# Kernel tuning notes

Hardware: AMD Instinct MI355X
Metric: run time of the kernel (lower is better)

The kernel has to match this reference:

```python
import jax, jax.numpy as jnp
import numpy as np

B, S, D, H, L, FF = 4, 2048, 256, 8, 4, 512
DK = D // H
EPS = 1e-5


def _ln(x, scale, bias):
    m = jnp.mean(x, axis=-1, keepdims=True)
    v = jnp.mean(jnp.square(x - m), axis=-1, keepdims=True)
    return (x - m) / jnp.sqrt(v + EPS) * scale + bias


def setup_inputs() -> dict:
    key = jax.random.key(0)
    ks = jax.random.split(key, 12)
    w = lambda k, shape: jax.random.normal(k, shape, dtype=jnp.float32) * 0.02
    return {
        "x": jax.random.normal(ks[0], (B, S, D), dtype=jnp.float32),
        "ln0_s": jnp.ones((D,), jnp.float32), "ln0_b": jnp.zeros((D,), jnp.float32),
        "ln1_s": jnp.ones((L, D), jnp.float32), "ln1_b": jnp.zeros((L, D), jnp.float32),
        "ln2_s": jnp.ones((L, D), jnp.float32), "ln2_b": jnp.zeros((L, D), jnp.float32),
        "wq": w(ks[1], (L, D, D)), "bq": jnp.zeros((L, D), jnp.float32),
        "wk": w(ks[2], (L, D, D)), "bk": jnp.zeros((L, D), jnp.float32),
        "wv": w(ks[3], (L, D, D)), "bv": jnp.zeros((L, D), jnp.float32),
        "wo": w(ks[4], (L, D, D)), "bo": jnp.zeros((L, D), jnp.float32),
        "w1": w(ks[5], (L, D, FF)), "b1": jnp.zeros((L, FF), jnp.float32),
        "w2": w(ks[6], (L, FF, D)), "b2": jnp.zeros((L, D), jnp.float32),
    }


def reference(x, ln0_s, ln0_b, ln1_s, ln1_b, ln2_s, ln2_b,
              wq, bq, wk, bk, wv, bv, wo, bo, w1, b1, w2, b2):
    scale = 1.0 / np.sqrt(DK).astype(np.float32)
    x = _ln(x, ln0_s, ln0_b)  # Encoder's leading LayerNorm

    def step(h, p):
        (l1s, l1b, l2s, l2b, Wq, Bq, Wk, Bk, Wv, Bv, Wo, Bo, W1, B1, W2, B2) = p
        # --- pre-norm multi-head attention ---
        x2 = _ln(h, l1s, l1b)
        q = (x2 @ Wq + Bq).reshape(B, S, H, DK)
        k = (x2 @ Wk + Bk).reshape(B, S, H, DK)
        v = (x2 @ Wv + Bv).reshape(B, S, H, DK)
        scores = jnp.einsum('bqhd,bkhd->bhqk', q, k) * scale  # [B,H,S,S]
        attn = jax.nn.softmax(scores, axis=-1)
        o = jnp.einsum('bhqk,bkhd->bqhd', attn, v).reshape(B, S, D)
        h = h + (o @ Wo + Bo)
        # --- pre-norm feed-forward (hidden fixed at 512, ReLU) ---
        x2 = _ln(h, l2s, l2b)
        h = h + (jax.nn.relu(x2 @ W1 + B1) @ W2 + B2)
        return h, None

    layer_params = (ln1_s, ln1_b, ln2_s, ln2_b, wq, bq, wk, bk,
                    wv, bv, wo, bo, w1, b1, w2, b2)
    x, _ = jax.lax.scan(step, x, layer_params)
    return x
```

## Files before the change

kernel.cpp:

```cpp
#include <hip/hip_runtime.h>
#include <hip/hip_bf16.h>
#include <math.h>

#define SEQ 2048
#define DIM 256
#define NH 8
#define DK 32
#define FF 512

typedef __bf16 bf16_t;
typedef bf16_t bf16x8 __attribute__((ext_vector_type(8)));
typedef bf16_t bf16x4 __attribute__((ext_vector_type(4)));
typedef float f32x4 __attribute__((ext_vector_type(4)));

#define QK_SCALE_LOG2 0.25503226632462494f
#if __has_builtin(__builtin_amdgcn_exp2f)
#define FAST_EXP2(x) __builtin_amdgcn_exp2f(x)
#else
#define FAST_EXP2(x) __expf((x) * 0.6931471805599453f)
#endif

__global__ __launch_bounds__(256) void ln_double_kernel(
    const float* __restrict__ x, const float* __restrict__ s0,
    const float* __restrict__ b0, const float* __restrict__ s1,
    const float* __restrict__ b1, float* __restrict__ outf,
    bf16_t* __restrict__ outb) {
  int wave = threadIdx.x >> 6;
  int lane = threadIdx.x & 63;
  int row = blockIdx.x * 4 + wave;
  float4 xv = *(const float4*)(x + (size_t)row * DIM + lane * 4);
  float sum = xv.x + xv.y + xv.z + xv.w;
  float sq = xv.x * xv.x + xv.y * xv.y + xv.z * xv.z + xv.w * xv.w;
#pragma unroll
  for (int off = 1; off < 64; off <<= 1) {
    sum += __shfl_xor(sum, off);
    sq += __shfl_xor(sq, off);
  }
  float mean = sum * (1.0f / 256.0f);
  float var = sq * (1.0f / 256.0f) - mean * mean;
  float inv = rsqrtf(var + 1e-5f);
  float4 sv = *(const float4*)(s0 + lane * 4);
  float4 bv = *(const float4*)(b0 + lane * 4);
  float4 h;
  h.x = (xv.x - mean) * inv * sv.x + bv.x;
  h.y = (xv.y - mean) * inv * sv.y + bv.y;
  h.z = (xv.z - mean) * inv * sv.z + bv.z;
  h.w = (xv.w - mean) * inv * sv.w + bv.w;
  *(float4*)(outf + (size_t)row * DIM + lane * 4) = h;
  float sum2 = h.x + h.y + h.z + h.w;
  float sq2 = h.x * h.x + h.y * h.y + h.z * h.z + h.w * h.w;
#pragma unroll
  for (int off = 1; off < 64; off <<= 1) {
    sum2 += __shfl_xor(sum2, off);
    sq2 += __shfl_xor(sq2, off);
  }
  float mean2 = sum2 * (1.0f / 256.0f);
  float var2 = sq2 * (1.0f / 256.0f) - mean2 * mean2;
  float inv2 = rsqrtf(var2 + 1e-5f);
  float4 s1v = *(const float4*)(s1 + lane * 4);
  float4 b1v = *(const float4*)(b1 + lane * 4);
  bf16x4 ob = {(bf16_t)((h.x - mean2) * inv2 * s1v.x + b1v.x),
               (bf16_t)((h.y - mean2) * inv2 * s1v.y + b1v.y),
               (bf16_t)((h.z - mean2) * inv2 * s1v.z + b1v.z),
               (bf16_t)((h.w - mean2) * inv2 * s1v.w + b1v.w)};
  *(bf16x4*)(outb + (size_t)row * DIM + lane * 4) = ob;
}

__global__ __launch_bounds__(256) void wtrans_all_kernel(
    const float* __restrict__ wq, const float* __restrict__ wk,
    const float* __restrict__ wv, const float* __restrict__ wo,
    const float* __restrict__ w1, const float* __restrict__ w2,
    bf16_t* __restrict__ WqT, bf16_t* __restrict__ WkT,
    bf16_t* __restrict__ WvT, bf16_t* __restrict__ WoT,
    bf16_t* __restrict__ W1T, bf16_t* __restrict__ W2T) {
  __shared__ float tile[64][65];
  int idx = blockIdx.x;
  int layer = idx >> 7;
  int r = idx & 127;
  const float* src;
  bf16_t* dst;
  int N, k0, n0;
  if (r < 64) {
    int which = r >> 4, t = r & 15;
    N = 256;
    k0 = (t & 3) * 64;
    n0 = (t >> 2) * 64;
    src = (which == 0 ? wq : which == 1 ? wk : which == 2 ? wv : wo) + (size_t)layer * 65536;
    dst = (which == 0 ? WqT : which == 1 ? WkT : which == 2 ? WvT : WoT) + (size_t)layer * 65536;
  } else if (r < 96) {
    int t = r - 64;
    N = 512;
    k0 = (t & 3) * 64;
    n0 = (t >> 2) * 64;
    src = w1 + (size_t)layer * 131072;
    dst = W1T + (size_t)layer * 131072;
  } else {
    int t = r - 96;
    N = 256;
    k0 = (t & 7) * 64;
    n0 = (t >> 3) * 64;
    src = w2 + (size_t)layer * 131072;
    dst = W2T + (size_t)layer * 131072;
  }
  int K = (r >= 96) ? 512 : 256;

  int tr = threadIdx.x >> 4;
  int tc4 = (threadIdx.x & 15) * 4;
#pragma unroll
  for (int i = 0; i < 4; i++) {
    int kl = i * 16 + tr;
    float4 v = *(const float4*)(src + (size_t)(k0 + kl) * N + n0 + tc4);
    tile[kl][tc4 + 0] = v.x; tile[kl][tc4 + 1] = v.y;
    tile[kl][tc4 + 2] = v.z; tile[kl][tc4 + 3] = v.w;
  }
  __syncthreads();
#pragma unroll
  for (int i = 0; i < 4; i++) {
    int nl = i * 16 + tr;
    bf16x4 o = {(bf16_t)tile[tc4 + 0][nl], (bf16_t)tile[tc4 + 1][nl],
                (bf16_t)tile[tc4 + 2][nl], (bf16_t)tile[tc4 + 3][nl]};
    *(bf16x4*)(dst + (size_t)(n0 + nl) * K + k0 + tc4) = o;
  }
}

__device__ __forceinline__ void stage128(const bf16_t* __restrict__ src,
                                         bf16_t* dst, int tid, int ldk, int k0) {
#pragma unroll
  for (int u = 0; u < 4; u++) {
    int i = u * 256 + tid;
    int m = i >> 3, cd = i & 7, cs = cd ^ (m & 7);
    __builtin_amdgcn_global_load_lds(
        (const __attribute__((address_space(1))) unsigned int*)(src + (size_t)m * ldk + k0 + cs * 8),
        (__attribute__((address_space(3))) unsigned int*)(dst + i * 8), 16, 0, 0);
  }
}

__device__ __forceinline__ void stage256(const bf16_t* __restrict__ src,
                                         bf16_t* dst, int tid, int ldk, int k0) {
#pragma unroll
  for (int u = 0; u < 8; u++) {
    int j = u * 256 + tid;
    int m = j >> 3, cd = j & 7, cs = cd ^ (m & 7);
    __builtin_amdgcn_global_load_lds(
        (const __attribute__((address_space(1))) unsigned int*)(src + (size_t)m * ldk + k0 + cs * 8),
        (__attribute__((address_space(3))) unsigned int*)(dst + j * 8), 16, 0, 0);
  }
}

__device__ __forceinline__ void compute128(const bf16_t* As, const bf16_t* Bs,
                                           int wr, int wc, int n16, int quad,
                                           f32x4 (&acc)[4][4]) {
#pragma unroll
  for (int ks = 0; ks < 2; ks++) {
    bf16x8 af[4], bf[4];
#pragma unroll
    for (int mt = 0; mt < 4; mt++) {
      int row = wr * 64 + mt * 16 + n16;
      int cd = (ks * 4 + quad) ^ (row & 7);
      af[mt] = *(const bf16x8*)(As + row * 64 + cd * 8);
    }
#pragma unroll
    for (int nt = 0; nt < 4; nt++) {
      int row = wc * 64 + nt * 16 + n16;
      int cd = (ks * 4 + quad) ^ (row & 7);
      bf[nt] = *(const bf16x8*)(Bs + row * 64 + cd * 8);
    }
#pragma unroll
    for (int mt = 0; mt < 4; mt++)
#pragma unroll
      for (int nt = 0; nt < 4; nt++)
        acc[mt][nt] = __builtin_amdgcn_mfma_f32_16x16x32_bf16(
            af[mt], bf[nt], acc[mt][nt], 0, 0, 0);
  }
}

template <int K>
__device__ __forceinline__ void gemm9_body(
    const bf16_t* __restrict__ A, const bf16_t* __restrict__ BT,
    int m0, int n0, int tid, bf16_t* As, bf16_t* Bs, f32x4 (&acc)[4][4]) {
  int lane = tid & 63;
  int n16 = lane & 15, quad = lane >> 4;
  int w = tid >> 6;
  int wr = w >> 1, wc = w & 1;
  const bf16_t* Arow = A + (size_t)m0 * K;
  const bf16_t* Brow = BT + (size_t)n0 * K;

  stage128(Arow, As, tid, K, 0);
  stage128(Brow, Bs, tid, K, 0);

  const int steps = K / 64;
#pragma unroll
  for (int s = 0; s < steps; s++) {
    int buf = s & 1;
    if (s + 1 < steps) {
      stage128(Arow, As + (buf ^ 1) * 8192, tid, K, (s + 1) * 64);
      stage128(Brow, Bs + (buf ^ 1) * 8192, tid, K, (s + 1) * 64);
    }
    __syncthreads();
    compute128(As + buf * 8192, Bs + buf * 8192, wr, wc, n16, quad, acc);
    if (s + 2 < steps) __syncthreads();
  }
}

__global__ __launch_bounds__(256) void qkv9_kernel(
    const bf16_t* __restrict__ A,
    const bf16_t* __restrict__ WqT, const bf16_t* __restrict__ WkT,
    const bf16_t* __restrict__ WvT,
    const float* __restrict__ bq, const float* __restrict__ bk,
    const float* __restrict__ bv,
    bf16_t* __restrict__ qo, bf16_t* __restrict__ ko,
    bf16_t* __restrict__ vo) {
  __shared__ __align__(16) bf16_t As[2 * 8192];
  __shared__ __align__(16) bf16_t Bs[2 * 8192];
  int which = blockIdx.x >> 1;
  int nblk = blockIdx.x & 1;
  const bf16_t* BT = (which == 0) ? WqT : (which == 1) ? WkT : WvT;
  const float* bias = (which == 0) ? bq : (which == 1) ? bk : bv;

  int tid = threadIdx.x;
  int lane = tid & 63;
  int n16 = lane & 15, quad = lane >> 4;
  int w = tid >> 6;
  int wr = w >> 1, wc = w & 1;
  int m0 = blockIdx.y * 128, n0 = nblk * 128;
  f32x4 acc[4][4] = {};
  gemm9_body<256>(A, BT, m0, n0, tid, As, Bs, acc);

#pragma unroll
  for (int nt = 0; nt < 4; nt++) {
    int n = n0 + wc * 64 + nt * 16 + n16;
    float bv_ = bias[n];
    int hh = n >> 5, dk = n & 31;
#pragma unroll
    for (int mt = 0; mt < 4; mt++) {
      if (which == 2) {
        int s0 = m0 + wr * 64 + mt * 16 + quad * 4;
        int bb = s0 >> 11, ss0 = s0 & 2047;
        bf16x4 o;
#pragma unroll
        for (int r = 0; r < 4; r++) o[r] = (bf16_t)(acc[mt][nt][r] + bv_);
        *(bf16x4*)(vo + ((size_t)(bb * NH + hh) * DK + dk) * SEQ + ss0) = o;
      } else {
        bf16_t* dst = (which == 0) ? qo : ko;
        float sc = (which == 0) ? QK_SCALE_LOG2 : 1.0f;
#pragma unroll
        for (int r = 0; r < 4; r++) {
          int m = m0 + wr * 64 + mt * 16 + quad * 4 + r;
          int bb = m >> 11, ss = m & 2047;
          dst[((size_t)(bb * NH + hh) * SEQ + ss) * DK + dk] =
              (bf16_t)((acc[mt][nt][r] + bv_) * sc);
        }
      }
    }
  }
}

template <int K, int LNOUT>
__global__ __launch_bounds__(256) void gemm_ln_kernel(
    const bf16_t* __restrict__ A, const bf16_t* __restrict__ BT,
    const float* __restrict__ bias, const float* __restrict__ resid,
    float* __restrict__ outf, const float* __restrict__ ls,
    const float* __restrict__ lb, bf16_t* __restrict__ outb) {
  __shared__ __align__(16) bf16_t As[2 * 2048];
  __shared__ __align__(16) bf16_t Bs[2 * 16384];
  __shared__ float2 stats[4][32];
  int tid = threadIdx.x;
  int lane = tid & 63;
  int n16 = lane & 15, quad = lane >> 4;
  int w = tid >> 6;
  int m0 = blockIdx.x * 32;

  const bf16_t* Arow = A + (size_t)m0 * K;
  f32x4 acc[2][4] = {};

  {
    int i = tid;
    int m = i >> 3, cd = i & 7, cs = cd ^ (m & 7);
    __builtin_amdgcn_global_load_lds(
        (const __attribute__((address_space(1))) unsigned int*)(Arow + (size_t)m * K + cs * 8),
        (__attribute__((address_space(3))) unsigned int*)(As + i * 8), 16, 0, 0);
    stage256(BT, Bs, tid, K, 0);
  }

  const int steps = K / 64;
#pragma unroll
  for (int s = 0; s < steps; s++) {
    int buf = s & 1;
    if (s + 1 < steps) {
      int k0 = (s + 1) * 64;
      int i = tid;
      int m = i >> 3, cd = i & 7, cs = cd ^ (m & 7);
      __builtin_amdgcn_global_load_lds(
          (const __attribute__((address_space(1))) unsigned int*)(Arow + (size_t)m * K + k0 + cs * 8),
          (__attribute__((address_space(3))) unsigned int*)(As + (buf ^ 1) * 2048 + i * 8), 16, 0, 0);
      stage256(BT, Bs + (buf ^ 1) * 16384, tid, K, k0);
    }
    __syncthreads();
    const bf16_t* a = As + buf * 2048;
    const bf16_t* b = Bs + buf * 16384;
#pragma unroll
    for (int ks = 0; ks < 2; ks++) {
      bf16x8 af[2], bfv[4];
#pragma unroll
      for (int mt = 0; mt < 2; mt++) {
        int row = mt * 16 + n16;
        int cd = (ks * 4 + quad) ^ (row & 7);
        af[mt] = *(const bf16x8*)(a + row * 64 + cd * 8);
      }
#pragma unroll
      for (int nt = 0; nt < 4; nt++) {
        int row = w * 64 + nt * 16 + n16;
        int cd = (ks * 4 + quad) ^ (row & 7);
        bfv[nt] = *(const bf16x8*)(b + row * 64 + cd * 8);
      }
#pragma unroll
      for (int mt = 0; mt < 2; mt++)
#pragma unroll
        for (int nt = 0; nt < 4; nt++)
          acc[mt][nt] = __builtin_amdgcn_mfma_f32_16x16x32_bf16(
              af[mt], bfv[nt], acc[mt][nt], 0, 0, 0);
    }
    if (s + 2 < steps) __syncthreads();
  }

  float rsum[2][4], rsq[2][4];
#pragma unroll
  for (int mt = 0; mt < 2; mt++)
#pragma unroll
    for (int r = 0; r < 4; r++) { rsum[mt][r] = 0.f; rsq[mt][r] = 0.f; }

#pragma unroll
  for (int nt = 0; nt < 4; nt++) {
    int n = w * 64 + nt * 16 + n16;
    float bv = bias[n];
#pragma unroll
    for (int mt = 0; mt < 2; mt++)
#pragma unroll
      for (int r = 0; r < 4; r++) {
        int m = m0 + mt * 16 + quad * 4 + r;
        size_t idx = (size_t)m * DIM + n;
        float hv = resid[idx] + acc[mt][nt][r] + bv;
        outf[idx] = hv;
        acc[mt][nt][r] = hv;
        rsum[mt][r] += hv;
        rsq[mt][r] += hv * hv;
      }
  }

  if (LNOUT) {
#pragma unroll
    for (int mt = 0; mt < 2; mt++)
#pragma unroll
      for (int r = 0; r < 4; r++) {
        float s_ = rsum[mt][r], q_ = rsq[mt][r];
#pragma unroll
        for (int off = 1; off < 16; off <<= 1) {
          s_ += __shfl_xor(s_, off);
          q_ += __shfl_xor(q_, off);
        }
        rsum[mt][r] = s_;
        rsq[mt][r] = q_;
      }
    if (n16 == 0) {
#pragma unroll
      for (int mt = 0; mt < 2; mt++)
#pragma unroll
        for (int r = 0; r < 4; r++)
          stats[w][mt * 16 + quad * 4 + r] = make_float2(rsum[mt][r], rsq[mt][r]);
    }
    __syncthreads();
#pragma unroll
    for (int mt = 0; mt < 2; mt++)
#pragma unroll
      for (int r = 0; r < 4; r++) {
        int lr = mt * 16 + quad * 4 + r;
        float2 t0 = stats[0][lr], t1 = stats[1][lr], t2 = stats[2][lr], t3 = stats[3][lr];
        float tot = t0.x + t1.x + t2.x + t3.x;
        float totq = t0.y + t1.y + t2.y + t3.y;
        float mean = tot * (1.0f / 256.0f);
        float var = totq * (1.0f / 256.0f) - mean * mean;
        rsum[mt][r] = mean;
        rsq[mt][r] = rsqrtf(var + 1e-5f);
      }
#pragma unroll
    for (int nt = 0; nt < 4; nt++) {
      int n = w * 64 + nt * 16 + n16;
      float sv = ls[n], bv = lb[n];
#pragma unroll
      for (int mt = 0; mt < 2; mt++)
#pragma unroll
        for (int r = 0; r < 4; r++) {
          int m = m0 + mt * 16 + quad * 4 + r;
          float x2 = (acc[mt][nt][r] - rsum[mt][r]) * rsq[mt][r] * sv + bv;
          outb[(size_t)m * DIM + n] = (bf16_t)x2;
        }
    }
  }
}

template <int LNOUT>
__global__ __launch_bounds__(256) void ffn_kernel(
    const bf16_t* __restrict__ x2, const bf16_t* __restrict__ W1T,
    const bf16_t* __restrict__ W2T, const float* __restrict__ b1,
    const float* __restrict__ b2, const float* __restrict__ resid,
    float* __restrict__ outf, const float* __restrict__ ls,
    const float* __restrict__ lb, bf16_t* __restrict__ outb) {
  __shared__ __align__(16) bf16_t Wbuf[2][16384];
  __shared__ __align__(16) bf16_t H1s[32 * 512];
  __shared__ float2 stats[4][32];
  int tid = threadIdx.x;
  int lane = tid & 63;
  int n16 = lane & 15, quad = lane >> 4;
  int w = tid >> 6;
  int m0 = blockIdx.x * 32;

#pragma unroll
  for (int s = 0; s < 2; s++) {
    const bf16_t* Wsrc = W1T + (size_t)s * 256 * 256;
    f32x4 acc_a[4][2] = {};
    stage256(Wsrc, Wbuf[0], tid, 256, 0);
#pragma unroll
    for (int t = 0; t < 4; t++) {
      int buf = t & 1;
      if (t + 1 < 4) stage256(Wsrc, Wbuf[buf ^ 1], tid, 256, (t + 1) * 64);
      __syncthreads();
#pragma unroll
      for (int ks = 0; ks < 2; ks++) {
        bf16x8 af[4];
#pragma unroll
        for (int mt = 0; mt < 4; mt++) {
          int row = w * 64 + mt * 16 + n16;
          int cd = (ks * 4 + quad) ^ (row & 7);
          af[mt] = *(const bf16x8*)(Wbuf[buf] + row * 64 + cd * 8);
        }
        bf16x8 xf[2];
#pragma unroll
        for (int nt = 0; nt < 2; nt++)
          xf[nt] = *(const bf16x8*)(x2 + (size_t)(m0 + nt * 16 + n16) * 256 +
                                    t * 64 + ks * 32 + quad * 8);
#pragma unroll
        for (int mt = 0; mt < 4; mt++)
#pragma unroll
          for (int nt = 0; nt < 2; nt++)
            acc_a[mt][nt] = __builtin_amdgcn_mfma_f32_16x16x32_bf16(
                af[mt], xf[nt], acc_a[mt][nt], 0, 0, 0);
      }
      __syncthreads();
    }
#pragma unroll
    for (int mt = 0; mt < 4; mt++) {
      int hid0 = s * 256 + w * 64 + mt * 16 + quad * 4;
      float b1v0 = b1[hid0], b1v1 = b1[hid0 + 1], b1v2 = b1[hid0 + 2], b1v3 = b1[hid0 + 3];
      int c = hid0 >> 3;
      int off4 = (quad & 1) * 4;
#pragma unroll
      for (int nt = 0; nt < 2; nt++) {
        int tok = nt * 16 + n16;
        bf16x4 o = {(bf16_t)fmaxf(acc_a[mt][nt][0] + b1v0, 0.0f),
                    (bf16_t)fmaxf(acc_a[mt][nt][1] + b1v1, 0.0f),
                    (bf16_t)fmaxf(acc_a[mt][nt][2] + b1v2, 0.0f),
                    (bf16_t)fmaxf(acc_a[mt][nt][3] + b1v3, 0.0f)};
        int cs = c ^ (n16 & 7);
        *(bf16x4*)(H1s + tok * 512 + cs * 8 + off4) = o;
      }
    }
  }
  __syncthreads();

  f32x4 acc[2][4] = {};
  stage256(W2T, Wbuf[0], tid, 512, 0);
#pragma unroll
  for (int s = 0; s < 8; s++) {
    int buf = s & 1;
    if (s + 1 < 8) stage256(W2T, Wbuf[buf ^ 1], tid, 512, (s + 1) * 64);
    __syncthreads();
#pragma unroll
    for (int ks = 0; ks < 2; ks++) {
      bf16x8 af2[2];
#pragma unroll
      for (int mt = 0; mt < 2; mt++) {
        int tok = mt * 16 + n16;
        int g = (s * 8 + ks * 4 + quad) ^ (n16 & 7);
        af2[mt] = *(const bf16x8*)(H1s + tok * 512 + g * 8);
      }
      bf16x8 bf2[4];
#pragma unroll
      for (int nt = 0; nt < 4; nt++) {
        int rowb = w * 64 + nt * 16 + n16;
        int cd = (ks * 4 + quad) ^ (rowb & 7);
        bf2[nt] = *(const bf16x8*)(Wbuf[buf] + rowb * 64 + cd * 8);
      }
#pragma unroll
      for (int mt = 0; mt < 2; mt++)
#pragma unroll
        for (int nt = 0; nt < 4; nt++)
          acc[mt][nt] = __builtin_amdgcn_mfma_f32_16x16x32_bf16(
              af2[mt], bf2[nt], acc[mt][nt], 0, 0, 0);
    }
    __syncthreads();
  }

  float rsum[2][4], rsq[2][4];
#pragma unroll
  for (int mt = 0; mt < 2; mt++)
#pragma unroll
    for (int r = 0; r < 4; r++) { rsum[mt][r] = 0.f; rsq[mt][r] = 0.f; }

#pragma unroll
  for (int nt = 0; nt < 4; nt++) {
    int n = w * 64 + nt * 16 + n16;
    float bv = b2[n];
#pragma unroll
    for (int mt = 0; mt < 2; mt++)
#pragma unroll
      for (int r = 0; r < 4; r++) {
        int m = m0 + mt * 16 + quad * 4 + r;
        size_t idx = (size_t)m * DIM + n;
        float hv = resid[idx] + acc[mt][nt][r] + bv;
        outf[idx] = hv;
        acc[mt][nt][r] = hv;
        rsum[mt][r] += hv;
        rsq[mt][r] += hv * hv;
      }
  }

  if (LNOUT) {
#pragma unroll
    for (int mt = 0; mt < 2; mt++)
#pragma unroll
      for (int r = 0; r < 4; r++) {
        float s_ = rsum[mt][r], q_ = rsq[mt][r];
#pragma unroll
        for (int off = 1; off < 16; off <<= 1) {
          s_ += __shfl_xor(s_, off);
          q_ += __shfl_xor(q_, off);
        }
        rsum[mt][r] = s_;
        rsq[mt][r] = q_;
      }
    if (n16 == 0) {
#pragma unroll
      for (int mt = 0; mt < 2; mt++)
#pragma unroll
        for (int r = 0; r < 4; r++)
          stats[w][mt * 16 + quad * 4 + r] = make_float2(rsum[mt][r], rsq[mt][r]);
    }
    __syncthreads();
#pragma unroll
    for (int mt = 0; mt < 2; mt++)
#pragma unroll
      for (int r = 0; r < 4; r++) {
        int lr = mt * 16 + quad * 4 + r;
        float2 t0 = stats[0][lr], t1 = stats[1][lr], t2 = stats[2][lr], t3 = stats[3][lr];
        float tot = t0.x + t1.x + t2.x + t3.x;
        float totq = t0.y + t1.y + t2.y + t3.y;
        float mean = tot * (1.0f / 256.0f);
        float var = totq * (1.0f / 256.0f) - mean * mean;
        rsum[mt][r] = mean;
        rsq[mt][r] = rsqrtf(var + 1e-5f);
      }
#pragma unroll
    for (int nt = 0; nt < 4; nt++) {
      int n = w * 64 + nt * 16 + n16;
      float sv = ls[n], bv = lb[n];
#pragma unroll
      for (int mt = 0; mt < 2; mt++)
#pragma unroll
        for (int r = 0; r < 4; r++) {
          int m = m0 + mt * 16 + quad * 4 + r;
          float x2v = (acc[mt][nt][r] - rsum[mt][r]) * rsq[mt][r] * sv + bv;
          outb[(size_t)m * DIM + n] = (bf16_t)x2v;
        }
    }
  }
}

__global__ __launch_bounds__(128) void flash8_kernel(
    const bf16_t* __restrict__ Q, const bf16_t* __restrict__ K,
    const bf16_t* __restrict__ VT, bf16_t* __restrict__ OB) {
  __shared__ __align__(16) bf16_t Plds[2][2][32][72];
  int bh = blockIdx.x;
  int q0 = blockIdx.y * 64;
  int w = threadIdx.x >> 6;
  int lane = threadIdx.x & 63;
  int n16 = lane & 15;
  int quad = lane >> 4;

  const bf16_t* Qb = Q + (size_t)bh * SEQ * DK;
  const bf16_t* Kb = K + (size_t)bh * SEQ * DK;
  const bf16_t* Vb = VT + (size_t)bh * DK * SEQ;
  int qr0 = q0 + w * 32;

  bf16x8 qfrag[2];
#pragma unroll
  for (int qg = 0; qg < 2; qg++)
    qfrag[qg] = *(const bf16x8*)(Qb + (size_t)(qr0 + qg * 16 + n16) * DK + quad * 8);

  bf16_t one = (bf16_t)1.0f;
  bf16x8 ones = {one, one, one, one, one, one, one, one};

  f32x4 oacc[2][2] = {};
  f32x4 lacc[2] = {};

  {
    bf16x8 kf0[4];
#pragma unroll
    for (int t = 0; t < 4; t++)
      kf0[t] = *(const bf16x8*)(Kb + (size_t)(t * 16 + n16) * DK + quad * 8);
#pragma unroll
    for (int qg = 0; qg < 2; qg++)
#pragma unroll
      for (int t = 0; t < 4; t++) {
        f32x4 sc = __builtin_amdgcn_mfma_f32_16x16x32_bf16(
            kf0[t], qfrag[qg], (f32x4){0.f, 0.f, 0.f, 0.f}, 0, 0, 0);
        bf16x4 pf;
#pragma unroll
        for (int r = 0; r < 4; r++) pf[r] = (bf16_t)FAST_EXP2(sc[r]);
        *(bf16x4*)&Plds[0][w][qg * 16 + n16][t * 16 + quad * 4] = pf;
      }
  }
  bf16x8 kfS[4], vfP[2][2];
#pragma unroll
  for (int t = 0; t < 4; t++)
    kfS[t] = *(const bf16x8*)(Kb + (size_t)(64 + t * 16 + n16) * DK + quad * 8);
#pragma unroll
  for (int c = 0; c < 2; c++) {
    vfP[c][0] = *(const bf16x8*)(Vb + (size_t)n16 * SEQ + c * 32 + quad * 8);
    vfP[c][1] = *(const bf16x8*)(Vb + (size_t)(16 + n16) * SEQ + c * 32 + quad * 8);
  }

#pragma unroll 2
  for (int i = 0; i < 32; i++) {
    int buf = i & 1;
    bf16x8 pf8[2][2];
#pragma unroll
    for (int qg = 0; qg < 2; qg++)
#pragma unroll
      for (int c = 0; c < 2; c++)
        pf8[qg][c] = *(const bf16x8*)&Plds[buf][w][qg * 16 + n16][c * 32 + quad * 8];
    bf16x8 kfN[4], vfN[2][2];
    if (i + 2 < 32) {
      int kb = (i + 2) * 64;
#pragma unroll
      for (int t = 0; t < 4; t++)
        kfN[t] = *(const bf16x8*)(Kb + (size_t)(kb + t * 16 + n16) * DK + quad * 8);
    }
    if (i + 1 < 32) {
      int kb = (i + 1) * 64;
#pragma unroll
      for (int c = 0; c < 2; c++) {
        vfN[c][0] = *(const bf16x8*)(Vb + (size_t)n16 * SEQ + kb + c * 32 + quad * 8);
        vfN[c][1] = *(const bf16x8*)(Vb + (size_t)(16 + n16) * SEQ + kb + c * 32 + quad * 8);
      }
    }
    if (i + 1 < 32) {
#pragma unroll
      for (int qg = 0; qg < 2; qg++)
#pragma unroll
        for (int t = 0; t < 4; t++) {
          f32x4 sc = __builtin_amdgcn_mfma_f32_16x16x32_bf16(
              kfS[t], qfrag[qg], (f32x4){0.f, 0.f, 0.f, 0.f}, 0, 0, 0);
          bf16x4 pf;
#pragma unroll
          for (int r = 0; r < 4; r++) pf[r] = (bf16_t)FAST_EXP2(sc[r]);
          *(bf16x4*)&Plds[buf ^ 1][w][qg * 16 + n16][t * 16 + quad * 4] = pf;
        }
    }
#pragma unroll
    for (int qg = 0; qg < 2; qg++)
#pragma unroll
      for (int c = 0; c < 2; c++) {
        lacc[qg] = __builtin_amdgcn_mfma_f32_16x16x32_bf16(pf8[qg][c], ones, lacc[qg], 0, 0, 0);
        oacc[qg][0] = __builtin_amdgcn_mfma_f32_16x16x32_bf16(pf8[qg][c], vfP[c][0], oacc[qg][0], 0, 0, 0);
        oacc[qg][1] = __builtin_amdgcn_mfma_f32_16x16x32_bf16(pf8[qg][c], vfP[c][1], oacc[qg][1], 0, 0, 0);
      }
    if (i + 2 < 32) {
#pragma unroll
      for (int t = 0; t < 4; t++) kfS[t] = kfN[t];
    }
    if (i + 1 < 32) {
#pragma unroll
      for (int c = 0; c < 2; c++) {
        vfP[c][0] = vfN[c][0];
        vfP[c][1] = vfN[c][1];
      }
    }
  }

  int bb = bh >> 3, hh = bh & 7;
#pragma unroll
  for (int qg = 0; qg < 2; qg++)
#pragma unroll
    for (int r = 0; r < 4; r++) {
      float linv = 1.0f / lacc[qg][r];
      int row = qr0 + qg * 16 + quad * 4 + r;
      bf16_t* op = OB + ((size_t)(bb * SEQ + row)) * DIM + hh * DK;
      op[n16] = (bf16_t)(oacc[qg][0][r] * linv);
      op[16 + n16] = (bf16_t)(oacc[qg][1][r] * linv);
    }
}

extern "C" void kernel_launch(void* const* d_in, const int* in_sizes, int n_in,
                              void* d_out, int out_size, void* d_ws, size_t ws_size,
                              hipStream_t stream) {
  const float* x     = (const float*)d_in[0];
  const float* ln0_s = (const float*)d_in[1];
  const float* ln0_b = (const float*)d_in[2];
  const float* ln1_s = (const float*)d_in[3];
  const float* ln1_b = (const float*)d_in[4];
  const float* ln2_s = (const float*)d_in[5];
  const float* ln2_b = (const float*)d_in[6];
  const float* wq = (const float*)d_in[7];
  const float* bq = (const float*)d_in[8];
  const float* wk = (const float*)d_in[9];
  const float* bk = (const float*)d_in[10];
  const float* wv = (const float*)d_in[11];
  const float* bv = (const float*)d_in[12];
  const float* wo = (const float*)d_in[13];
  const float* bo = (const float*)d_in[14];
  const float* w1 = (const float*)d_in[15];
  const float* b1 = (const float*)d_in[16];
  const float* w2 = (const float*)d_in[17];
  const float* b2 = (const float*)d_in[18];

  float* out = (float*)d_out;
  const size_t ACT = (size_t)8192 * DIM;

  bf16_t* wsb = (bf16_t*)d_ws;
  bf16_t* x2b = wsb;
  bf16_t* obf = x2b + ACT;
  bf16_t* qbf = obf + ACT;
  bf16_t* kbf = qbf + ACT;
  bf16_t* vbf = kbf + ACT;
  bf16_t* WqT = vbf + ACT;
  bf16_t* WkT = WqT + 4 * 65536;
  bf16_t* WvT = WkT + 4 * 65536;
  bf16_t* WoT = WvT + 4 * 65536;
  bf16_t* W1T = WoT + 4 * 65536;
  bf16_t* W2T = W1T + 4 * 131072;

  dim3 blk(256);
  dim3 blkF(128);
  dim3 gLN(2048);
  dim3 gRow(256);
  dim3 gQKV(6, 64);
  dim3 gAtt(32, 32);

  wtrans_all_kernel<<<dim3(512), blk, 0, stream>>>(wq, wk, wv, wo, w1, w2,
                                                   WqT, WkT, WvT, WoT, W1T, W2T);

  ln_double_kernel<<<gLN, blk, 0, stream>>>(x, ln0_s, ln0_b, ln1_s, ln1_b, out, x2b);

  for (int l = 0; l < 4; l++) {
    bf16_t* WqTl = WqT + (size_t)l * 65536;
    bf16_t* WkTl = WkT + (size_t)l * 65536;
    bf16_t* WvTl = WvT + (size_t)l * 65536;
    bf16_t* WoTl = WoT + (size_t)l * 65536;
    bf16_t* W1Tl = W1T + (size_t)l * 131072;
    bf16_t* W2Tl = W2T + (size_t)l * 131072;

    qkv9_kernel<<<gQKV, blk, 0, stream>>>(x2b, WqTl, WkTl, WvTl,
                                          bq + l * DIM, bk + l * DIM, bv + l * DIM,
                                          qbf, kbf, vbf);
    flash8_kernel<<<gAtt, blkF, 0, stream>>>(qbf, kbf, vbf, obf);
    gemm_ln_kernel<256, 1><<<gRow, blk, 0, stream>>>(
        obf, WoTl, bo + l * DIM, out, out, ln2_s + l * DIM, ln2_b + l * DIM, x2b);
    if (l < 3) {
      ffn_kernel<1><<<gRow, blk, 0, stream>>>(
          x2b, W1Tl, W2Tl, b1 + l * FF, b2 + l * DIM, out, out,
          ln1_s + (l + 1) * DIM, ln1_b + (l + 1) * DIM, x2b);
    } else {
      ffn_kernel<0><<<gRow, blk, 0, stream>>>(
          x2b, W1Tl, W2Tl, b1 + l * FF, b2 + l * DIM, out, out,
          nullptr, nullptr, nullptr);
    }
  }
}
```

Measured before the change: 453.0 us.

## Split attention key range across two blocks and combine partial results

```diff
diff --git a/kernel.cpp b/kernel.cpp
--- a/kernel.cpp
+++ b/kernel.cpp
@@ -575,20 +575,22 @@
   }
 }
 
-__global__ __launch_bounds__(128) void flash8_kernel(
+__global__ __launch_bounds__(128, 4) void flash9_kernel(
     const bf16_t* __restrict__ Q, const bf16_t* __restrict__ K,
-    const bf16_t* __restrict__ VT, bf16_t* __restrict__ OB) {
+    const bf16_t* __restrict__ VT, float* __restrict__ Opart,
+    float* __restrict__ lpart) {
   __shared__ __align__(16) bf16_t Plds[2][2][32][72];
   int bh = blockIdx.x;
   int q0 = blockIdx.y * 64;
+  int part = blockIdx.z;
   int w = threadIdx.x >> 6;
   int lane = threadIdx.x & 63;
   int n16 = lane & 15;
   int quad = lane >> 4;
 
   const bf16_t* Qb = Q + (size_t)bh * SEQ * DK;
-  const bf16_t* Kb = K + (size_t)bh * SEQ * DK;
-  const bf16_t* Vb = VT + (size_t)bh * DK * SEQ;
+  const bf16_t* Kb = K + (size_t)bh * SEQ * DK + (size_t)part * 1024 * DK;
+  const bf16_t* Vb = VT + (size_t)bh * DK * SEQ + part * 1024;
   int qr0 = q0 + w * 32;
 
   bf16x8 qfrag[2];
@@ -630,7 +632,7 @@
   }
 
 #pragma unroll 2
-  for (int i = 0; i < 32; i++) {
+  for (int i = 0; i < 16; i++) {
     int buf = i & 1;
     bf16x8 pf8[2][2];
 #pragma unroll
@@ -639,13 +641,13 @@
       for (int c = 0; c < 2; c++)
         pf8[qg][c] = *(const bf16x8*)&Plds[buf][w][qg * 16 + n16][c * 32 + quad * 8];
     bf16x8 kfN[4], vfN[2][2];
-    if (i + 2 < 32) {
+    if (i + 2 < 16) {
       int kb = (i + 2) * 64;
 #pragma unroll
       for (int t = 0; t < 4; t++)
         kfN[t] = *(const bf16x8*)(Kb + (size_t)(kb + t * 16 + n16) * DK + quad * 8);
     }
-    if (i + 1 < 32) {
+    if (i + 1 < 16) {
       int kb = (i + 1) * 64;
 #pragma unroll
       for (int c = 0; c < 2; c++) {
@@ -653,7 +655,7 @@
         vfN[c][1] = *(const bf16x8*)(Vb + (size_t)(16 + n16) * SEQ + kb + c * 32 + quad * 8);
       }
     }
-    if (i + 1 < 32) {
+    if (i + 1 < 16) {
 #pragma unroll
       for (int qg = 0; qg < 2; qg++)
 #pragma unroll
@@ -674,11 +676,11 @@
         oacc[qg][0] = __builtin_amdgcn_mfma_f32_16x16x32_bf16(pf8[qg][c], vfP[c][0], oacc[qg][0], 0, 0, 0);
         oacc[qg][1] = __builtin_amdgcn_mfma_f32_16x16x32_bf16(pf8[qg][c], vfP[c][1], oacc[qg][1], 0, 0, 0);
       }
-    if (i + 2 < 32) {
+    if (i + 2 < 16) {
 #pragma unroll
       for (int t = 0; t < 4; t++) kfS[t] = kfN[t];
     }
-    if (i + 1 < 32) {
+    if (i + 1 < 16) {
 #pragma unroll
       for (int c = 0; c < 2; c++) {
         vfP[c][0] = vfN[c][0];
@@ -687,17 +689,34 @@
     }
   }
 
+  size_t rowbase = (size_t)part * 65536 + (size_t)bh * SEQ;
+#pragma unroll
+  for (int qg = 0; qg < 2; qg++) {
+#pragma unroll
+    for (int r = 0; r < 4; r++) {
+      int row = qr0 + qg * 16 + quad * 4 + r;
+      float* op = Opart + (rowbase + row) * 32;
+      op[n16] = oacc[qg][0][r];
+      op[16 + n16] = oacc[qg][1][r];
+      if (n16 == 0) lpart[rowbase + row] = lacc[qg][r];
+    }
+  }
+}
+
+__global__ __launch_bounds__(256) void combine_kernel(
+    const float* __restrict__ Opart, const float* __restrict__ lpart,
+    bf16_t* __restrict__ OB) {
+  int g = blockIdx.x * 256 + threadIdx.x;
+  int row = g >> 3;
+  int dk0 = (g & 7) * 4;
+  float4 o0 = *(const float4*)(Opart + (size_t)row * 32 + dk0);
+  float4 o1 = *(const float4*)(Opart + (size_t)(65536 + row) * 32 + dk0);
+  float linv = 1.0f / (lpart[row] + lpart[65536 + row]);
+  int bh = row >> 11, s = row & 2047;
   int bb = bh >> 3, hh = bh & 7;
-#pragma unroll
-  for (int qg = 0; qg < 2; qg++)
-#pragma unroll
-    for (int r = 0; r < 4; r++) {
-      float linv = 1.0f / lacc[qg][r];
-      int row = qr0 + qg * 16 + quad * 4 + r;
-      bf16_t* op = OB + ((size_t)(bb * SEQ + row)) * DIM + hh * DK;
-      op[n16] = (bf16_t)(oacc[qg][0][r] * linv);
-      op[16 + n16] = (bf16_t)(oacc[qg][1][r] * linv);
-    }
+  bf16x4 o = {(bf16_t)((o0.x + o1.x) * linv), (bf16_t)((o0.y + o1.y) * linv),
+              (bf16_t)((o0.z + o1.z) * linv), (bf16_t)((o0.w + o1.w) * linv)};
+  *(bf16x4*)(OB + ((size_t)(bb * SEQ + s)) * DIM + hh * DK + dk0) = o;
 }
 
 extern "C" void kernel_launch(void* const* d_in, const int* in_sizes, int n_in,
@@ -738,13 +757,16 @@
   bf16_t* WoT = WvT + 4 * 65536;
   bf16_t* W1T = WoT + 4 * 65536;
   bf16_t* W2T = W1T + 4 * 131072;
+  float* Opart = (float*)(W2T + 4 * 131072);
+  float* lpart = Opart + (size_t)2 * 65536 * 32;
 
   dim3 blk(256);
   dim3 blkF(128);
   dim3 gLN(2048);
   dim3 gRow(256);
   dim3 gQKV(6, 64);
-  dim3 gAtt(32, 32);
+  dim3 gAtt(32, 32, 2);
+  dim3 gComb(2048);
 
   wtrans_all_kernel<<<dim3(512), blk, 0, stream>>>(wq, wk, wv, wo, w1, w2,
                                                    WqT, WkT, WvT, WoT, W1T, W2T);
@@ -762,7 +784,8 @@
     qkv9_kernel<<<gQKV, blk, 0, stream>>>(x2b, WqTl, WkTl, WvTl,
                                           bq + l * DIM, bk + l * DIM, bv + l * DIM,
                                           qbf, kbf, vbf);
-    flash8_kernel<<<gAtt, blkF, 0, stream>>>(qbf, kbf, vbf, obf);
+    flash9_kernel<<<gAtt, blkF, 0, stream>>>(qbf, kbf, vbf, Opart, lpart);
+    combine_kernel<<<gComb, blk, 0, stream>>>(Opart, lpart, obf);
     gemm_ln_kernel<256, 1><<<gRow, blk, 0, stream>>>(
         obf, WoTl, bo + l * DIM, out, out, ln2_s + l * DIM, ln2_b + l * DIM, x2b);
     if (l < 3) {
```

Result: slower. 543.3 us (+19.9%).

## Fuse output projection, LayerNorm and FFN into one per-row tail kernel

Applied to the files above, without the earlier changes.

```diff
diff --git a/kernel.cpp b/kernel.cpp
--- a/kernel.cpp
+++ b/kernel.cpp
@@ -255,92 +255,246 @@
   }
 }
 
-template <int K, int LNOUT>
-__global__ __launch_bounds__(256) void gemm_ln_kernel(
-    const bf16_t* __restrict__ A, const bf16_t* __restrict__ BT,
-    const float* __restrict__ bias, const float* __restrict__ resid,
-    float* __restrict__ outf, const float* __restrict__ ls,
-    const float* __restrict__ lb, bf16_t* __restrict__ outb) {
-  __shared__ __align__(16) bf16_t As[2 * 2048];
-  __shared__ __align__(16) bf16_t Bs[2 * 16384];
+template <int LNOUT>
+__global__ __launch_bounds__(256) void tail_kernel(
+    const bf16_t* __restrict__ O, const bf16_t* __restrict__ WoT,
+    const float* __restrict__ bo, const bf16_t* __restrict__ W1T,
+    const bf16_t* __restrict__ W2T, const float* __restrict__ b1,
+    const float* __restrict__ b2, const float* __restrict__ ls2,
+    const float* __restrict__ lb2, float* __restrict__ outf,
+    const float* __restrict__ ls1n, const float* __restrict__ lb1n,
+    bf16_t* __restrict__ outb) {
+  __shared__ __align__(16) bf16_t Wbuf[2][16384];
+  __shared__ __align__(16) bf16_t H1s[32 * 512];
+  __shared__ __align__(16) bf16_t X2s[32 * 264];
   __shared__ float2 stats[4][32];
   int tid = threadIdx.x;
   int lane = tid & 63;
   int n16 = lane & 15, quad = lane >> 4;
   int w = tid >> 6;
   int m0 = blockIdx.x * 32;
-
-  const bf16_t* Arow = A + (size_t)m0 * K;
-  f32x4 acc[2][4] = {};
-
+  bf16_t* As = H1s;
+
+  f32x4 hreg[2][4] = {};
   {
-    int i = tid;
-    int m = i >> 3, cd = i & 7, cs = cd ^ (m & 7);
-    __builtin_amdgcn_global_load_lds(
-        (const __attribute__((address_space(1))) unsigned int*)(Arow + (size_t)m * K + cs * 8),
-        (__attribute__((address_space(3))) unsigned int*)(As + i * 8), 16, 0, 0);
-    stage256(BT, Bs, tid, K, 0);
-  }
-
-  const int steps = K / 64;
-#pragma unroll
-  for (int s = 0; s < steps; s++) {
-    int buf = s & 1;
-    if (s + 1 < steps) {
-      int k0 = (s + 1) * 64;
+    const bf16_t* Arow = O + (size_t)m0 * 256;
+    {
       int i = tid;
       int m = i >> 3, cd = i & 7, cs = cd ^ (m & 7);
       __builtin_amdgcn_global_load_lds(
-          (const __attribute__((address_space(1))) unsigned int*)(Arow + (size_t)m * K + k0 + cs * 8),
-          (__attribute__((address_space(3))) unsigned int*)(As + (buf ^ 1) * 2048 + i * 8), 16, 0, 0);
-      stage256(BT, Bs + (buf ^ 1) * 16384, tid, K, k0);
-    }
+          (const __attribute__((address_space(1))) unsigned int*)(Arow + (size_t)m * 256 + cs * 8),
+          (__attribute__((address_space(3))) unsigned int*)(As + i * 8), 16, 0, 0);
+      stage256(WoT, Wbuf[0], tid, 256, 0);
+    }
+#pragma unroll
+    for (int s = 0; s < 4; s++) {
+      int buf = s & 1;
+      if (s + 1 < 4) {
+        int k0 = (s + 1) * 64;
+        int i = tid;
+        int m = i >> 3, cd = i & 7, cs = cd ^ (m & 7);
+        __builtin_amdgcn_global_load_lds(
+            (const __attribute__((address_space(1))) unsigned int*)(Arow + (size_t)m * 256 + k0 + cs * 8),
+            (__attribute__((address_space(3))) unsigned int*)(As + (buf ^ 1) * 2048 + i * 8), 16, 0, 0);
+        stage256(WoT, Wbuf[buf ^ 1], tid, 256, k0);
+      }
+      __syncthreads();
+      const bf16_t* a = As + buf * 2048;
+      const bf16_t* b = Wbuf[buf];
+#pragma unroll
+      for (int ks = 0; ks < 2; ks++) {
+        bf16x8 af[2], bfv[4];
+#pragma unroll
+        for (int mt = 0; mt < 2; mt++) {
+          int row = mt * 16 + n16;
+          int cd = (ks * 4 + quad) ^ (row & 7);
+          af[mt] = *(const bf16x8*)(a + row * 64 + cd * 8);
+        }
+#pragma unroll
+        for (int nt = 0; nt < 4; nt++) {
+          int row = w * 64 + nt * 16 + n16;
+          int cd = (ks * 4 + quad) ^ (row & 7);
+          bfv[nt] = *(const bf16x8*)(b + row * 64 + cd * 8);
+        }
+#pragma unroll
+        for (int mt = 0; mt < 2; mt++)
+#pragma unroll
+          for (int nt = 0; nt < 4; nt++)
+            hreg[mt][nt] = __builtin_amdgcn_mfma_f32_16x16x32_bf16(
+                af[mt], bfv[nt], hreg[mt][nt], 0, 0, 0);
+      }
+      __syncthreads();
+    }
+  }
+
+  float rsum[2][4], rsq[2][4];
+#pragma unroll
+  for (int mt = 0; mt < 2; mt++)
+#pragma unroll
+    for (int r = 0; r < 4; r++) { rsum[mt][r] = 0.f; rsq[mt][r] = 0.f; }
+#pragma unroll
+  for (int nt = 0; nt < 4; nt++) {
+    int n = w * 64 + nt * 16 + n16;
+    float bv = bo[n];
+#pragma unroll
+    for (int mt = 0; mt < 2; mt++)
+#pragma unroll
+      for (int r = 0; r < 4; r++) {
+        int m = m0 + mt * 16 + quad * 4 + r;
+        float hv = outf[(size_t)m * DIM + n] + hreg[mt][nt][r] + bv;
+        hreg[mt][nt][r] = hv;
+        rsum[mt][r] += hv;
+        rsq[mt][r] += hv * hv;
+      }
+  }
+#pragma unroll
+  for (int mt = 0; mt < 2; mt++)
+#pragma unroll
+    for (int r = 0; r < 4; r++) {
+      float s_ = rsum[mt][r], q_ = rsq[mt][r];
+#pragma unroll
+      for (int off = 1; off < 16; off <<= 1) {
+        s_ += __shfl_xor(s_, off);
+        q_ += __shfl_xor(q_, off);
+      }
+      rsum[mt][r] = s_;
+      rsq[mt][r] = q_;
+    }
+  if (n16 == 0) {
+#pragma unroll
+    for (int mt = 0; mt < 2; mt++)
+#pragma unroll
+      for (int r = 0; r < 4; r++)
+        stats[w][mt * 16 + quad * 4 + r] = make_float2(rsum[mt][r], rsq[mt][r]);
+  }
+  __syncthreads();
+#pragma unroll
+  for (int mt = 0; mt < 2; mt++)
+#pragma unroll
+    for (int r = 0; r < 4; r++) {
+      int lr = mt * 16 + quad * 4 + r;
+      float2 t0 = stats[0][lr], t1 = stats[1][lr], t2 = stats[2][lr], t3 = stats[3][lr];
+      float tot = t0.x + t1.x + t2.x + t3.x;
+      float totq = t0.y + t1.y + t2.y + t3.y;
+      float mean = tot * (1.0f / 256.0f);
+      float var = totq * (1.0f / 256.0f) - mean * mean;
+      rsum[mt][r] = mean;
+      rsq[mt][r] = rsqrtf(var + 1e-5f);
+    }
+#pragma unroll
+  for (int nt = 0; nt < 4; nt++) {
+    int n = w * 64 + nt * 16 + n16;
+    float sv = ls2[n], bv = lb2[n];
+#pragma unroll
+    for (int mt = 0; mt < 2; mt++)
+#pragma unroll
+      for (int r = 0; r < 4; r++) {
+        int rl = mt * 16 + quad * 4 + r;
+        X2s[rl * 264 + n] = (bf16_t)((hreg[mt][nt][r] - rsum[mt][r]) * rsq[mt][r] * sv + bv);
+      }
+  }
+  __syncthreads();
+
+#pragma unroll
+  for (int s = 0; s < 2; s++) {
+    const bf16_t* Wsrc = W1T + (size_t)s * 256 * 256;
+    f32x4 acc_a[4][2] = {};
+    stage256(Wsrc, Wbuf[0], tid, 256, 0);
+#pragma unroll
+    for (int t = 0; t < 4; t++) {
+      int buf = t & 1;
+      if (t + 1 < 4) stage256(Wsrc, Wbuf[buf ^ 1], tid, 256, (t + 1) * 64);
+      __syncthreads();
+#pragma unroll
+      for (int ks = 0; ks < 2; ks++) {
+        bf16x8 af[4];
+#pragma unroll
+        for (int mt = 0; mt < 4; mt++) {
+          int row = w * 64 + mt * 16 + n16;
+          int cd = (ks * 4 + quad) ^ (row & 7);
+          af[mt] = *(const bf16x8*)(Wbuf[buf] + row * 64 + cd * 8);
+        }
+        bf16x8 xf[2];
+#pragma unroll
+        for (int nt = 0; nt < 2; nt++)
+          xf[nt] = *(const bf16x8*)(X2s + (nt * 16 + n16) * 264 + t * 64 + ks * 32 + quad * 8);
+#pragma unroll
+        for (int mt = 0; mt < 4; mt++)
+#pragma unroll
+          for (int nt = 0; nt < 2; nt++)
+            acc_a[mt][nt] = __builtin_amdgcn_mfma_f32_16x16x32_bf16(
+                af[mt], xf[nt], acc_a[mt][nt], 0, 0, 0);
+      }
+      __syncthreads();
+    }
+#pragma unroll
+    for (int mt = 0; mt < 4; mt++) {
+      int hid0 = s * 256 + w * 64 + mt * 16 + quad * 4;
+      float b1v0 = b1[hid0], b1v1 = b1[hid0 + 1], b1v2 = b1[hid0 + 2], b1v3 = b1[hid0 + 3];
+      int c = hid0 >> 3;
+      int off4 = (quad & 1) * 4;
+#pragma unroll
+      for (int nt = 0; nt < 2; nt++) {
+        int tok = nt * 16 + n16;
+        bf16x4 o = {(bf16_t)fmaxf(acc_a[mt][nt][0] + b1v0, 0.0f),
+                    (bf16_t)fmaxf(acc_a[mt][nt][1] + b1v1, 0.0f),
+                    (bf16_t)fmaxf(acc_a[mt][nt][2] + b1v2, 0.0f),
+                    (bf16_t)fmaxf(acc_a[mt][nt][3] + b1v3, 0.0f)};
+        int cs = c ^ (n16 & 7);
+        *(bf16x4*)(H1s + tok * 512 + cs * 8 + off4) = o;
+      }
+    }
+  }
+  __syncthreads();
+
+  f32x4 acc[2][4] = {};
+  stage256(W2T, Wbuf[0], tid, 512, 0);
+#pragma unroll
+  for (int s = 0; s < 8; s++) {
+    int buf = s & 1;
+    if (s + 1 < 8) stage256(W2T, Wbuf[buf ^ 1], tid, 512, (s + 1) * 64);
     __syncthreads();
-    const bf16_t* a = As + buf * 2048;
-    const bf16_t* b = Bs + buf * 16384;
 #pragma unroll
     for (int ks = 0; ks < 2; ks++) {
-      bf16x8 af[2], bfv[4];
+      bf16x8 af2[2];
 #pragma unroll
       for (int mt = 0; mt < 2; mt++) {
-        int row = mt * 16 + n16;
-        int cd = (ks * 4 + quad) ^ (row & 7);
-        af[mt] = *(const bf16x8*)(a + row * 64 + cd * 8);
-      }
+        int tok = mt * 16 + n16;
+        int g = (s * 8 + ks * 4 + quad) ^ (n16 & 7);
+        af2[mt] = *(const bf16x8*)(H1s + tok * 512 + g * 8);
+      }
+      bf16x8 bf2[4];
 #pragma unroll
       for (int nt = 0; nt < 4; nt++) {
-        int row = w * 64 + nt * 16 + n16;
-        int cd = (ks * 4 + quad) ^ (row & 7);
-        bfv[nt] = *(const bf16x8*)(b + row * 64 + cd * 8);
+        int rowb = w * 64 + nt * 16 + n16;
+        int cd = (ks * 4 + quad) ^ (rowb & 7);
+        bf2[nt] = *(const bf16x8*)(Wbuf[buf] + rowb * 64 + cd * 8);
       }
 #pragma unroll
       for (int mt = 0; mt < 2; mt++)
 #pragma unroll
         for (int nt = 0; nt < 4; nt++)
           acc[mt][nt] = __builtin_amdgcn_mfma_f32_16x16x32_bf16(
-              af[mt], bfv[nt], acc[mt][nt], 0, 0, 0);
-    }
-    if (s + 2 < steps) __syncthreads();
-  }
-
-  float rsum[2][4], rsq[2][4];
+              af2[mt], bf2[nt], acc[mt][nt], 0, 0, 0);
+    }
+    __syncthreads();
+  }
+
 #pragma unroll
   for (int mt = 0; mt < 2; mt++)
 #pragma unroll
     for (int r = 0; r < 4; r++) { rsum[mt][r] = 0.f; rsq[mt][r] = 0.f; }
-
 #pragma unroll
   for (int nt = 0; nt < 4; nt++) {
     int n = w * 64 + nt * 16 + n16;
-    float bv = bias[n];
+    float bv = b2[n];
 #pragma unroll
     for (int mt = 0; mt < 2; mt++)
 #pragma unroll
       for (int r = 0; r < 4; r++) {
         int m = m0 + mt * 16 + quad * 4 + r;
-        size_t idx = (size_t)m * DIM + n;
-        float hv = resid[idx] + acc[mt][nt][r] + bv;
-        outf[idx] = hv;
+        float hv = hreg[mt][nt][r] + acc[mt][nt][r] + bv;
+        outf[(size_t)m * DIM + n] = hv;
         acc[mt][nt][r] = hv;
         rsum[mt][r] += hv;
         rsq[mt][r] += hv * hv;
@@ -385,184 +539,7 @@
 #pragma unroll
     for (int nt = 0; nt < 4; nt++) {
       int n = w * 64 + nt * 16 + n16;
-      float sv = ls[n], bv = lb[n];
-#pragma unroll
-      for (int mt = 0; mt < 2; mt++)
-#pragma unroll
-        for (int r = 0; r < 4; r++) {
-          int m = m0 + mt * 16 + quad * 4 + r;
-          float x2 = (acc[mt][nt][r] - rsum[mt][r]) * rsq[mt][r] * sv + bv;
-          outb[(size_t)m * DIM + n] = (bf16_t)x2;
-        }
-    }
-  }
-}
-
-template <int LNOUT>
-__global__ __launch_bounds__(256) void ffn_kernel(
-    const bf16_t* __restrict__ x2, const bf16_t* __restrict__ W1T,
-    const bf16_t* __restrict__ W2T, const float* __restrict__ b1,
-    const float* __restrict__ b2, const float* __restrict__ resid,
-    float* __restrict__ outf, const float* __restrict__ ls,
-    const float* __restrict__ lb, bf16_t* __restrict__ outb) {
-  __shared__ __align__(16) bf16_t Wbuf[2][16384];
-  __shared__ __align__(16) bf16_t H1s[32 * 512];
-  __shared__ float2 stats[4][32];
-  int tid = threadIdx.x;
-  int lane = tid & 63;
-  int n16 = lane & 15, quad = lane >> 4;
-  int w = tid >> 6;
-  int m0 = blockIdx.x * 32;
-
-#pragma unroll
-  for (int s = 0; s < 2; s++) {
-    const bf16_t* Wsrc = W1T + (size_t)s * 256 * 256;
-    f32x4 acc_a[4][2] = {};
-    stage256(Wsrc, Wbuf[0], tid, 256, 0);
-#pragma unroll
-    for (int t = 0; t < 4; t++) {
-      int buf = t & 1;
-      if (t + 1 < 4) stage256(Wsrc, Wbuf[buf ^ 1], tid, 256, (t + 1) * 64);
-      __syncthreads();
-#pragma unroll
-      for (int ks = 0; ks < 2; ks++) {
-        bf16x8 af[4];
-#pragma unroll
-        for (int mt = 0; mt < 4; mt++) {
-          int row = w * 64 + mt * 16 + n16;
-          int cd = (ks * 4 + quad) ^ (row & 7);
-          af[mt] = *(const bf16x8*)(Wbuf[buf] + row * 64 + cd * 8);
-        }
-        bf16x8 xf[2];
-#pragma unroll
-        for (int nt = 0; nt < 2; nt++)
-          xf[nt] = *(const bf16x8*)(x2 + (size_t)(m0 + nt * 16 + n16) * 256 +
-                                    t * 64 + ks * 32 + quad * 8);
-#pragma unroll
-        for (int mt = 0; mt < 4; mt++)
-#pragma unroll
-          for (int nt = 0; nt < 2; nt++)
-            acc_a[mt][nt] = __builtin_amdgcn_mfma_f32_16x16x32_bf16(
-                af[mt], xf[nt], acc_a[mt][nt], 0, 0, 0);
-      }
-      __syncthreads();
-    }
-#pragma unroll
-    for (int mt = 0; mt < 4; mt++) {
-      int hid0 = s * 256 + w * 64 + mt * 16 + quad * 4;
-      float b1v0 = b1[hid0], b1v1 = b1[hid0 + 1], b1v2 = b1[hid0 + 2], b1v3 = b1[hid0 + 3];
-      int c = hid0 >> 3;
-      int off4 = (quad & 1) * 4;
-#pragma unroll
-      for (int nt = 0; nt < 2; nt++) {
-        int tok = nt * 16 + n16;
-        bf16x4 o = {(bf16_t)fmaxf(acc_a[mt][nt][0] + b1v0, 0.0f),
-                    (bf16_t)fmaxf(acc_a[mt][nt][1] + b1v1, 0.0f),
-                    (bf16_t)fmaxf(acc_a[mt][nt][2] + b1v2, 0.0f),
-                    (bf16_t)fmaxf(acc_a[mt][nt][3] + b1v3, 0.0f)};
-        int cs = c ^ (n16 & 7);
-        *(bf16x4*)(H1s + tok * 512 + cs * 8 + off4) = o;
-      }
-    }
-  }
-  __syncthreads();
-
-  f32x4 acc[2][4] = {};
-  stage256(W2T, Wbuf[0], tid, 512, 0);
-#pragma unroll
-  for (int s = 0; s < 8; s++) {
-    int buf = s & 1;
-    if (s + 1 < 8) stage256(W2T, Wbuf[buf ^ 1], tid, 512, (s + 1) * 64);
-    __syncthreads();
-#pragma unroll
-    for (int ks = 0; ks < 2; ks++) {
-      bf16x8 af2[2];
-#pragma unroll
-      for (int mt = 0; mt < 2; mt++) {
-        int tok = mt * 16 + n16;
-        int g = (s * 8 + ks * 4 + quad) ^ (n16 & 7);
-        af2[mt] = *(const bf16x8*)(H1s + tok * 512 + g * 8);
-      }
-      bf16x8 bf2[4];
-#pragma unroll
-      for (int nt = 0; nt < 4; nt++) {
-        int rowb = w * 64 + nt * 16 + n16;
-        int cd = (ks * 4 + quad) ^ (rowb & 7);
-        bf2[nt] = *(const bf16x8*)(Wbuf[buf] + rowb * 64 + cd * 8);
-      }
-#pragma unroll
-      for (int mt = 0; mt < 2; mt++)
-#pragma unroll
-        for (int nt = 0; nt < 4; nt++)
-          acc[mt][nt] = __builtin_amdgcn_mfma_f32_16x16x32_bf16(
-              af2[mt], bf2[nt], acc[mt][nt], 0, 0, 0);
-    }
-    __syncthreads();
-  }
-
-  float rsum[2][4], rsq[2][4];
-#pragma unroll
-  for (int mt = 0; mt < 2; mt++)
-#pragma unroll
-    for (int r = 0; r < 4; r++) { rsum[mt][r] = 0.f; rsq[mt][r] = 0.f; }
-
-#pragma unroll
-  for (int nt = 0; nt < 4; nt++) {
-    int n = w * 64 + nt * 16 + n16;
-    float bv = b2[n];
-#pragma unroll
-    for (int mt = 0; mt < 2; mt++)
-#pragma unroll
-      for (int r = 0; r < 4; r++) {
-        int m = m0 + mt * 16 + quad * 4 + r;
-        size_t idx = (size_t)m * DIM + n;
-        float hv = resid[idx] + acc[mt][nt][r] + bv;
-        outf[idx] = hv;
-        acc[mt][nt][r] = hv;
-        rsum[mt][r] += hv;
-        rsq[mt][r] += hv * hv;
-      }
-  }
-
-  if (LNOUT) {
-#pragma unroll
-    for (int mt = 0; mt < 2; mt++)
-#pragma unroll
-      for (int r = 0; r < 4; r++) {
-        float s_ = rsum[mt][r], q_ = rsq[mt][r];
-#pragma unroll
-        for (int off = 1; off < 16; off <<= 1) {
-          s_ += __shfl_xor(s_, off);
-          q_ += __shfl_xor(q_, off);
-        }
-        rsum[mt][r] = s_;
-        rsq[mt][r] = q_;
-      }
-    if (n16 == 0) {
-#pragma unroll
-      for (int mt = 0; mt < 2; mt++)
-#pragma unroll
-        for (int r = 0; r < 4; r++)
-          stats[w][mt * 16 + quad * 4 + r] = make_float2(rsum[mt][r], rsq[mt][r]);
-    }
-    __syncthreads();
-#pragma unroll
-    for (int mt = 0; mt < 2; mt++)
-#pragma unroll
-      for (int r = 0; r < 4; r++) {
-        int lr = mt * 16 + quad * 4 + r;
-        float2 t0 = stats[0][lr], t1 = stats[1][lr], t2 = stats[2][lr], t3 = stats[3][lr];
-        float tot = t0.x + t1.x + t2.x + t3.x;
-        float totq = t0.y + t1.y + t2.y + t3.y;
-        float mean = tot * (1.0f / 256.0f);
-        float var = totq * (1.0f / 256.0f) - mean * mean;
-        rsum[mt][r] = mean;
-        rsq[mt][r] = rsqrtf(var + 1e-5f);
-      }
-#pragma unroll
-    for (int nt = 0; nt < 4; nt++) {
-      int n = w * 64 + nt * 16 + n16;
-      float sv = ls[n], bv = lb[n];
+      float sv = ls1n[n], bv = lb1n[n];
 #pragma unroll
       for (int mt = 0; mt < 2; mt++)
 #pragma unroll
@@ -763,15 +740,15 @@
                                           bq + l * DIM, bk + l * DIM, bv + l * DIM,
                                           qbf, kbf, vbf);
     flash8_kernel<<<gAtt, blkF, 0, stream>>>(qbf, kbf, vbf, obf);
-    gemm_ln_kernel<256, 1><<<gRow, blk, 0, stream>>>(
-        obf, WoTl, bo + l * DIM, out, out, ln2_s + l * DIM, ln2_b + l * DIM, x2b);
     if (l < 3) {
-      ffn_kernel<1><<<gRow, blk, 0, stream>>>(
-          x2b, W1Tl, W2Tl, b1 + l * FF, b2 + l * DIM, out, out,
+      tail_kernel<1><<<gRow, blk, 0, stream>>>(
+          obf, WoTl, bo + l * DIM, W1Tl, W2Tl, b1 + l * FF, b2 + l * DIM,
+          ln2_s + l * DIM, ln2_b + l * DIM, out,
           ln1_s + (l + 1) * DIM, ln1_b + (l + 1) * DIM, x2b);
     } else {
-      ffn_kernel<0><<<gRow, blk, 0, stream>>>(
-          x2b, W1Tl, W2Tl, b1 + l * FF, b2 + l * DIM, out, out,
+      tail_kernel<0><<<gRow, blk, 0, stream>>>(
+          obf, WoTl, bo + l * DIM, W1Tl, W2Tl, b1 + l * FF, b2 + l * DIM,
+          ln2_s + l * DIM, ln2_b + l * DIM, out,
           nullptr, nullptr, nullptr);
     }
   }
```

After: 423.4 us. 1.07x faster.
